# Kernel tuning notes

Hardware: AMD Instinct MI355X
Metric: run time of the kernel (lower is better)

## Reference

```python
import jax, jax.numpy as jnp
import numpy as np

B, L, D, H = 2, 2048, 1024, 16
DH = D // H
TAU = 0.1


def setup_inputs() -> dict:
    key = jax.random.key(0)
    ks = jax.random.split(key, 12)
    s = 0.02
    return {
        "q_x": jax.random.normal(ks[0], (B, L, D), jnp.float32),
        "k_x": jax.random.normal(ks[1], (B, L, D), jnp.float32),
        "v_x": jax.random.normal(ks[2], (B, L, D), jnp.float32),
        "ec": jax.random.normal(ks[3], (B, L, D), jnp.float32),
        "Wq": jax.random.normal(ks[4], (D, D), jnp.float32) * s,
        "bq": jnp.zeros((D,), jnp.float32),
        "Wk": jax.random.normal(ks[5], (D, D), jnp.float32) * s,
        "bk": jnp.zeros((D,), jnp.float32),
        "Wv": jax.random.normal(ks[6], (D, D), jnp.float32) * s,
        "bv": jnp.zeros((D,), jnp.float32),
        "Wo": jax.random.normal(ks[7], (D, D), jnp.float32) * s,
        "bo": jnp.zeros((D,), jnp.float32),
    }


def reference(q_x, k_x, v_x, ec, Wq, bq, Wk, bk, Wv, bv, Wo, bo):
    # torch nn.Linear: y = x @ W.T + b
    Q = (q_x @ Wq.T + bq).reshape(B, L, H, DH).transpose(0, 2, 1, 3)   # [B,H,L,Dh]
    K = (k_x @ Wk.T + bk).reshape(B, -1, H, DH).transpose(0, 2, 1, 3)  # [B,H,S,Dh]
    V = (v_x @ Wv.T + bv).reshape(B, -1, H, DH).transpose(0, 2, 1, 3)  # [B,H,S,Dh]
    scores = jnp.einsum("bhld,bhsd->bhls", Q, K) / jnp.sqrt(jnp.float32(DH))
    w = jnp.nan_to_num(jax.nn.softmax(scores, axis=-1), nan=0.0)       # [B,H,L,S]
    # frequency gate per key position: sigmoid((mean|ec| - tau) * 10)
    gate = jax.nn.sigmoid((jnp.abs(ec).mean(-1) - TAU) * 10.0)          # [B,S]
    w = w * gate[:, None, None, :]
    out = jnp.einsum("bhls,bhsd->bhld", w, V)                           # [B,H,L,Dh]
    out = out.transpose(0, 2, 1, 3).reshape(B, L, D)
    return out @ Wo.T + bo
```

## Files before the change

kernel.cpp:

```cpp
#include <hip/hip_runtime.h>

typedef unsigned short u16;
typedef unsigned int u32;
typedef unsigned long long u64;
typedef __attribute__((ext_vector_type(8))) short bf16x8;
typedef __attribute__((ext_vector_type(4))) float f32x4;
typedef __attribute__((ext_vector_type(2))) unsigned int u32x2;
typedef __attribute__((ext_vector_type(4))) unsigned int u32x4;

#define B_ 2
#define L_ 2048
#define D_ 1024
#define H_ 16
#define M_ 4096

__device__ __forceinline__ u16 f2bf(float f) {
  u32 x = __builtin_bit_cast(u32, f);
  return (u16)((x + 0x7fffu + ((x >> 16) & 1u)) >> 16);
}
__device__ __forceinline__ u32 cvtpk(float lo, float hi) {
  u32 r;
  asm("v_cvt_pk_bf16_f32 %0, %1, %2" : "=v"(r) : "v"(lo), "v"(hi));
  return r;
}

__device__ __forceinline__ void lane_regroup(u32& a, u32& b) {
#if __has_builtin(__builtin_amdgcn_permlane32_swap) && \
    __has_builtin(__builtin_amdgcn_permlane16_swap)
  u32x2 r = __builtin_amdgcn_permlane32_swap(a, b, false, false);
  u32x2 t = __builtin_amdgcn_permlane16_swap(r.x, r.y, false, false);
  a = t.x;
  b = t.y;
#else
  asm("v_permlane32_swap_b32 %0, %1\n\t"
      "v_permlane16_swap_b32 %0, %1"
      : "+v"(a), "+v"(b));
#endif
}

__device__ __forceinline__ void gl2lds16(void* lds, const void* g) {
  __builtin_amdgcn_global_load_lds(
      (const __attribute__((address_space(1))) u32*)g,
      (__attribute__((address_space(3))) u32*)lds, 16, 0, 0);
}

__device__ __forceinline__ void wait_vm8() {
  asm volatile("s_waitcnt vmcnt(8)" ::: "memory");
}
__device__ __forceinline__ void wait_vm0() {
  asm volatile("s_waitcnt vmcnt(0)" ::: "memory");
}
__device__ __forceinline__ void bar() {
  asm volatile("" ::: "memory");
  __builtin_amdgcn_s_barrier();
  asm volatile("" ::: "memory");
}

__global__ void cvt_all(const float* __restrict__ q, const float* __restrict__ k,
                        const float* __restrict__ v, const float* __restrict__ wq,
                        const float* __restrict__ wk, const float* __restrict__ wv,
                        const float* __restrict__ wo, u16* __restrict__ Xq,
                        u16* __restrict__ Xk, u16* __restrict__ Xv, u16* __restrict__ Wqb,
                        u16* __restrict__ Wkb, u16* __restrict__ Wvb,
                        u16* __restrict__ Wob) {
  int i = blockIdx.x * 256 + threadIdx.x;
  const float* s;
  u16* d;
  int off;
  if (i < 3145728) {
    int t = i >> 20;
    off = i & 1048575;
    s = t == 0 ? q : t == 1 ? k : v;
    d = t == 0 ? Xq : t == 1 ? Xk : Xv;
  } else {
    int j = i - 3145728;
    int t = j >> 18;
    off = j & 262143;
    s = t == 0 ? wq : t == 1 ? wk : t == 2 ? wv : wo;
    d = t == 0 ? Wqb : t == 1 ? Wkb : t == 2 ? Wvb : Wob;
  }
  float4 vv = ((const float4*)s)[off];
  ((u64*)d)[off] = (u64)cvtpk(vv.x, vv.y) | ((u64)cvtpk(vv.z, vv.w) << 32);
}

__global__ void gate_kernel(const float* __restrict__ ec, float* __restrict__ gate) {
  int row = blockIdx.x * 4 + (threadIdx.x >> 6);
  int lane = threadIdx.x & 63;
  const float4* p = (const float4*)(ec + (size_t)row * 1024);
  float s = 0.f;
#pragma unroll
  for (int i = 0; i < 4; i++) {
    float4 v = p[i * 64 + lane];
    s += fabsf(v.x) + fabsf(v.y) + fabsf(v.z) + fabsf(v.w);
  }
#pragma unroll
  for (int m = 1; m < 64; m <<= 1) s += __shfl_xor(s, m);
  if (lane == 0) {
    float mean = s * (1.0f / 1024.0f);
    gate[row] = 1.0f / (1.0f + __expf(-(mean - 0.1f) * 10.0f));
  }
}

__global__ __launch_bounds__(256, 2) void gemm_qkv(
    const u16* __restrict__ Xq, const u16* __restrict__ Xk, const u16* __restrict__ Xv,
    const u16* __restrict__ Wq, const u16* __restrict__ Wk, const u16* __restrict__ Wv,
    const float* __restrict__ bq, const float* __restrict__ bk,
    const float* __restrict__ bv, const float* __restrict__ gate,
    u16* __restrict__ Qo, u16* __restrict__ Ko, u16* __restrict__ Vt) {
  __shared__ char smem[65536];
  const int which = blockIdx.x >> 8;
  const u16* A = which == 0 ? Xq : which == 1 ? Xk : Xv;
  const u16* Bw = which == 0 ? Wq : which == 1 ? Wk : Wv;
  const float* bias = which == 0 ? bq : which == 1 ? bk : bv;
  const int bi = blockIdx.x & 255;
  const int tid = threadIdx.x;
  const int tm = bi >> 3;
  const int tn = bi & 7;
  const int w = tid >> 6, lane = tid & 63;
  const int c = lane & 15, g = lane >> 4;
  const int wr = (w >> 1) << 6, wc = (w & 1) << 6;
  const int srow = tid >> 3, sch = tid & 7;

  f32x4 acc[4][4] = {};

  auto stage = [&](int buf, int t) {
    char* As = smem + buf * 32768;
    char* Bs = As + 16384;
#pragma unroll
    for (int i = 0; i < 4; i++) {
      int row = i * 32 + srow;
      int chs = (sch ^ (row & 7)) << 3;
      gl2lds16(As + i * 4096 + w * 1024, A + (size_t)(tm * 128 + row) * 1024 + t * 64 + chs);
      gl2lds16(Bs + i * 4096 + w * 1024, Bw + (size_t)(tn * 128 + row) * 1024 + t * 64 + chs);
    }
  };

  stage(0, 0);
  for (int t = 0; t < 16; t++) {
    int cur = t & 1;
    if (t < 15) {
      stage(cur ^ 1, t + 1);
      wait_vm8();
    } else {
      wait_vm0();
    }
    bar();
    const char* As = smem + cur * 32768;
    const char* Bs = As + 16384;
#pragma unroll
    for (int kd = 0; kd < 2; kd++) {
      bf16x8 af[4], bfr[4];
#pragma unroll
      for (int fi = 0; fi < 4; fi++) {
        int ra = wr + fi * 16 + c;
        af[fi] = *(const bf16x8*)(As + ra * 128 + ((((kd << 2) | g) ^ (ra & 7)) << 4));
        int rb = wc + fi * 16 + c;
        bfr[fi] = *(const bf16x8*)(Bs + rb * 128 + ((((kd << 2) | g) ^ (rb & 7)) << 4));
      }
#pragma unroll
      for (int fi = 0; fi < 4; fi++)
#pragma unroll
        for (int fj = 0; fj < 4; fj++)
          acc[fi][fj] = __builtin_amdgcn_mfma_f32_16x16x32_bf16(af[fi], bfr[fj],
                                                                acc[fi][fj], 0, 0, 0);
    }
    bar();
  }

  if (which == 2) {
    u16* T = (u16*)smem;
    __syncthreads();
#pragma unroll
    for (int fi = 0; fi < 4; fi++) {
      int lr0 = wr + fi * 16 + g * 4;
      float4 gg = *(const float4*)(gate + tm * 128 + lr0);
#pragma unroll
      for (int fj = 0; fj < 4; fj++) {
        int lc = wc + fj * 16 + c;
        float bv2 = bias[tn * 128 + lc];
        T[lc * 136 + lr0 + 0] = f2bf((acc[fi][fj][0] + bv2) * gg.x);
        T[lc * 136 + lr0 + 1] = f2bf((acc[fi][fj][1] + bv2) * gg.y);
        T[lc * 136 + lr0 + 2] = f2bf((acc[fi][fj][2] + bv2) * gg.z);
        T[lc * 136 + lr0 + 3] = f2bf((acc[fi][fj][3] + bv2) * gg.w);
      }
    }
    __syncthreads();
    const int lc = tid >> 1, hf = tid & 1;
    const int vtrow = (tm >> 4) * 1024 + tn * 128 + lc;
    const int s0 = (tm & 15) * 128 + hf * 64;
    const char* Trow = (const char*)(T + lc * 136) + hf * 128;
    u16* dst = Vt + (size_t)vtrow * 2048 + s0;
#pragma unroll
    for (int j = 0; j < 8; j++)
      *(bf16x8*)(dst + j * 8) = *(const bf16x8*)(Trow + j * 16);
  } else {
    u16* Cout = which == 0 ? Qo : Ko;
    const int rowb = tm * 128 + wr + g * 4;
    const int colb = tn * 128 + wc + c;
#pragma unroll
    for (int fj = 0; fj < 4; fj++) {
      int col = colb + fj * 16;
      float bv2 = bias[col];
#pragma unroll
      for (int fi = 0; fi < 4; fi++) {
        int r0 = rowb + fi * 16;
#pragma unroll
        for (int r = 0; r < 4; r++)
          Cout[(size_t)(r0 + r) * 1024 + col] = f2bf(acc[fi][fj][r] + bv2);
      }
    }
  }
}

__global__ __launch_bounds__(256, 2) void gemm_o(const u16* __restrict__ A,
                                                 const u16* __restrict__ Bw,
                                                 const float* __restrict__ bias,
                                                 float* __restrict__ Cout) {
  __shared__ char smem[65536];
  const int tid = threadIdx.x;
  const int tm = blockIdx.x >> 3;
  const int tn = blockIdx.x & 7;
  const int w = tid >> 6, lane = tid & 63;
  const int c = lane & 15, g = lane >> 4;
  const int wr = (w >> 1) << 6, wc = (w & 1) << 6;
  const int srow = tid >> 3, sch = tid & 7;

  f32x4 acc[4][4] = {};

  auto stage = [&](int buf, int t) {
    char* As = smem + buf * 32768;
    char* Bs = As + 16384;
#pragma unroll
    for (int i = 0; i < 4; i++) {
      int row = i * 32 + srow;
      int chs = (sch ^ (row & 7)) << 3;
      gl2lds16(As + i * 4096 + w * 1024, A + (size_t)(tm * 128 + row) * 1024 + t * 64 + chs);
      gl2lds16(Bs + i * 4096 + w * 1024, Bw + (size_t)(tn * 128 + row) * 1024 + t * 64 + chs);
    }
  };

  stage(0, 0);
  for (int t = 0; t < 16; t++) {
    int cur = t & 1;
    if (t < 15) {
      stage(cur ^ 1, t + 1);
      wait_vm8();
    } else {
      wait_vm0();
    }
    bar();
    const char* As = smem + cur * 32768;
    const char* Bs = As + 16384;
#pragma unroll
    for (int kd = 0; kd < 2; kd++) {
      bf16x8 af[4], bfr[4];
#pragma unroll
      for (int fi = 0; fi < 4; fi++) {
        int ra = wr + fi * 16 + c;
        af[fi] = *(const bf16x8*)(As + ra * 128 + ((((kd << 2) | g) ^ (ra & 7)) << 4));
        int rb = wc + fi * 16 + c;
        bfr[fi] = *(const bf16x8*)(Bs + rb * 128 + ((((kd << 2) | g) ^ (rb & 7)) << 4));
      }
#pragma unroll
      for (int fi = 0; fi < 4; fi++)
#pragma unroll
        for (int fj = 0; fj < 4; fj++)
          acc[fi][fj] = __builtin_amdgcn_mfma_f32_16x16x32_bf16(af[fi], bfr[fj],
                                                                acc[fi][fj], 0, 0, 0);
    }
    bar();
  }

  const int rowb = tm * 128 + wr + g * 4;
  const int colb = tn * 128 + wc + c;
#pragma unroll
  for (int fj = 0; fj < 4; fj++) {
    int col = colb + fj * 16;
    float bv2 = bias[col];
#pragma unroll
    for (int fi = 0; fi < 4; fi++) {
      int r0 = rowb + fi * 16;
#pragma unroll
      for (int r = 0; r < 4; r++)
        Cout[(size_t)(r0 + r) * 1024 + col] = acc[fi][fj][r] + bv2;
    }
  }
}

__global__ __launch_bounds__(256, 2) void attn_kernel(const u16* __restrict__ Qb,
                                                      const u16* __restrict__ Kb,
                                                      const u16* __restrict__ Vt,
                                                      u16* __restrict__ Ob) {
  __shared__ char asmem[65536];
  const int bi = blockIdx.x;
  const int bh = (bi & 7) | ((bi >> 7) << 3);
  const int qt = (bi >> 3) & 15;
  const int b = bh >> 4, h = bh & 15;
  const int tid = threadIdx.x, w = tid >> 6, lane = tid & 63;
  const int c = lane & 15, g = lane >> 4;
  const int qrow0 = b * L_ + qt * 128 + w * 32;
  const float SCL = 0.18033688011112042f;

  bf16x8 qf[2][2];
#pragma unroll
  for (int fj = 0; fj < 2; fj++)
#pragma unroll
    for (int kd = 0; kd < 2; kd++)
      qf[fj][kd] = *(const bf16x8*)(Qb + (size_t)(qrow0 + fj * 16 + c) * D_ + h * 64 +
                                    kd * 32 + g * 8);

  float lsum[2] = {0.f, 0.f};
  f32x4 oacc[4][2] = {};

  const int srow = tid >> 3, sch = tid & 7;
  const int vrow = tid >> 4, vch = tid & 15;

  auto stage = [&](int buf, int kv) {
    char* KsB = asmem + buf * 32768;
    char* VsB = KsB + 16384;
    int sbase = kv * 128;
#pragma unroll
    for (int i = 0; i < 4; i++) {
      int kr = i * 32 + srow;
      gl2lds16(KsB + i * 4096 + w * 1024,
               Kb + (size_t)(b * L_ + sbase + kr) * D_ + h * 64 + ((sch ^ (kr & 7)) << 3));
      int vr = i * 16 + vrow;
      gl2lds16(VsB + i * 4096 + w * 1024,
               Vt + (size_t)(bh * 64 + vr) * 2048 + sbase + ((vch ^ (vr & 15)) << 3));
    }
  };

  stage(0, 0);
  for (int kv = 0; kv < 16; kv++) {
    int cur = kv & 1;
    if (kv < 15) {
      stage(cur ^ 1, kv + 1);
      wait_vm8();
    } else {
      wait_vm0();
    }
    bar();
    const char* Ks = asmem + cur * 32768;
    const char* Vs = Ks + 16384;

#pragma unroll
    for (int fj = 0; fj < 2; fj++) {
      f32x4 st[8] = {};
#pragma unroll
      for (int kd = 0; kd < 2; kd++) {
#pragma unroll
        for (int fi = 0; fi < 8; fi++) {
          int row = fi * 16 + c;
          bf16x8 kf = *(const bf16x8*)(Ks + row * 128 + ((((kd << 2) | g) ^ (c & 7)) << 4));
          st[fi] = __builtin_amdgcn_mfma_f32_16x16x32_bf16(kf, qf[fj][kd], st[fi], 0, 0, 0);
        }
      }
      float rs = 0.f;
      u32 pkA[8], pkB[8];
#pragma unroll
      for (int fi = 0; fi < 8; fi++) {
        float p0 = __builtin_amdgcn_exp2f(st[fi][0] * SCL);
        float p1 = __builtin_amdgcn_exp2f(st[fi][1] * SCL);
        float p2 = __builtin_amdgcn_exp2f(st[fi][2] * SCL);
        float p3 = __builtin_amdgcn_exp2f(st[fi][3] * SCL);
        rs += (p0 + p1) + (p2 + p3);
        pkA[fi] = cvtpk(p0, p1);
        pkB[fi] = cvtpk(p2, p3);
      }
      rs += __shfl_xor(rs, 16);
      rs += __shfl_xor(rs, 32);
      lsum[fj] += rs;
#pragma unroll
      for (int ks = 0; ks < 4; ks++) {
        u32 a0 = pkA[2 * ks], b0 = pkA[2 * ks + 1];
        lane_regroup(a0, b0);
        u32 a1 = pkB[2 * ks], b1 = pkB[2 * ks + 1];
        lane_regroup(a1, b1);
        u32x4 pw = {a0, a1, b0, b1};
        bf16x8 pf = __builtin_bit_cast(bf16x8, pw);
#pragma unroll
        for (int fd = 0; fd < 4; fd++) {
          int vr2 = fd * 16 + c;
          bf16x8 vf = *(const bf16x8*)(Vs + vr2 * 256 + ((((ks << 2) | g) ^ (vr2 & 15)) << 4));
          oacc[fd][fj] = __builtin_amdgcn_mfma_f32_16x16x32_bf16(vf, pf, oacc[fd][fj],
                                                                 0, 0, 0);
        }
      }
    }
    bar();
  }

#pragma unroll
  for (int fj = 0; fj < 2; fj++) {
    float inv = 1.0f / lsum[fj];
    size_t orow = (size_t)(qrow0 + fj * 16 + c) * D_ + h * 64;
#pragma unroll
    for (int fd = 0; fd < 4; fd++) {
      u64 pk = (u64)cvtpk(oacc[fd][fj][0] * inv, oacc[fd][fj][1] * inv) |
               ((u64)cvtpk(oacc[fd][fj][2] * inv, oacc[fd][fj][3] * inv) << 32);
      *(u64*)(Ob + orow + fd * 16 + g * 4) = pk;
    }
  }
}

extern "C" void kernel_launch(void* const* d_in, const int* in_sizes, int n_in,
                              void* d_out, int out_size, void* d_ws, size_t ws_size,
                              hipStream_t stream) {
  const float* q_x = (const float*)d_in[0];
  const float* k_x = (const float*)d_in[1];
  const float* v_x = (const float*)d_in[2];
  const float* ec = (const float*)d_in[3];
  const float* Wq = (const float*)d_in[4];
  const float* bq = (const float*)d_in[5];
  const float* Wk = (const float*)d_in[6];
  const float* bk = (const float*)d_in[7];
  const float* Wv = (const float*)d_in[8];
  const float* bv = (const float*)d_in[9];
  const float* Wo = (const float*)d_in[10];
  const float* bo = (const float*)d_in[11];

  char* ws = (char*)d_ws;
  const size_t MB = 1024 * 1024;
  u16* Wqb = (u16*)(ws + 0 * MB);
  u16* Wkb = (u16*)(ws + 2 * MB);
  u16* Wvb = (u16*)(ws + 4 * MB);
  u16* Wob = (u16*)(ws + 6 * MB);
  float* gatep = (float*)(ws + 8 * MB);
  u16* Xq = (u16*)(ws + 9 * MB);
  u16* Xk = (u16*)(ws + 17 * MB);
  u16* Xv = (u16*)(ws + 25 * MB);
  u16* Qb = (u16*)(ws + 33 * MB);
  u16* Kb = (u16*)(ws + 41 * MB);
  u16* Vtb = (u16*)(ws + 49 * MB);
  u16* Ab = Xk;

  gate_kernel<<<1024, 256, 0, stream>>>(ec, gatep);
  cvt_all<<<16384, 256, 0, stream>>>(q_x, k_x, v_x, Wq, Wk, Wv, Wo, Xq, Xk, Xv, Wqb,
                                     Wkb, Wvb, Wob);
  gemm_qkv<<<768, 256, 0, stream>>>(Xq, Xk, Xv, Wqb, Wkb, Wvb, bq, bk, bv, gatep, Qb,
                                    Kb, Vtb);
  attn_kernel<<<512, 256, 0, stream>>>(Qb, Kb, Vtb, Ab);
  gemm_o<<<256, 256, 0, stream>>>(Ab, Wob, bo, (float*)d_out);
}
```

Baseline: 120.2 us.

## Shrink attention tiles to 64x64 and fold softmax scale into Q projection

The attention kernel now gives each wave 16 query rows instead of 32 and streams 64-key tiles instead of 128. Shared memory halves to 32KB and the grid doubles to 1024 blocks, with launch bounds raised to 4 blocks per CU to improve occupancy and latency hiding. The softmax scale (log2e/sqrt(dh)) is now applied in the Q projection epilogue, which removes a multiply per score element in the attention loop. Costs: K/V tiles are reloaded twice as often per query row, there are more barriers per unit of work, and Q is rounded to bf16 after scaling.

```diff
diff --git a/kernel.cpp b/kernel.cpp
--- a/kernel.cpp
+++ b/kernel.cpp
@@ -46,6 +46,9 @@
 
 __device__ __forceinline__ void wait_vm8() {
   asm volatile("s_waitcnt vmcnt(8)" ::: "memory");
+}
+__device__ __forceinline__ void wait_vm4() {
+  asm volatile("s_waitcnt vmcnt(4)" ::: "memory");
 }
 __device__ __forceinline__ void wait_vm0() {
   asm volatile("s_waitcnt vmcnt(0)" ::: "memory");
@@ -195,6 +198,7 @@
       *(bf16x8*)(dst + j * 8) = *(const bf16x8*)(Trow + j * 16);
   } else {
     u16* Cout = which == 0 ? Qo : Ko;
+    const float oscl = which == 0 ? 0.18033688011112042f : 1.0f;
     const int rowb = tm * 128 + wr + g * 4;
     const int colb = tn * 128 + wc + c;
 #pragma unroll
@@ -206,7 +210,7 @@
         int r0 = rowb + fi * 16;
 #pragma unroll
         for (int r = 0; r < 4; r++)
-          Cout[(size_t)(r0 + r) * 1024 + col] = f2bf(acc[fi][fj][r] + bv2);
+          Cout[(size_t)(r0 + r) * 1024 + col] = f2bf((acc[fi][fj][r] + bv2) * oscl);
       }
     }
   }
@@ -287,119 +291,106 @@
   }
 }
 
-__global__ __launch_bounds__(256, 2) void attn_kernel(const u16* __restrict__ Qb,
+__global__ __launch_bounds__(256, 4) void attn_kernel(const u16* __restrict__ Qb,
                                                       const u16* __restrict__ Kb,
                                                       const u16* __restrict__ Vt,
                                                       u16* __restrict__ Ob) {
-  __shared__ char asmem[65536];
+  __shared__ char asmem[32768];
   const int bi = blockIdx.x;
-  const int bh = (bi & 7) | ((bi >> 7) << 3);
-  const int qt = (bi >> 3) & 15;
+  const int bh = (bi & 7) | ((bi >> 8) << 3);
+  const int qt = (bi >> 3) & 31;
   const int b = bh >> 4, h = bh & 15;
   const int tid = threadIdx.x, w = tid >> 6, lane = tid & 63;
   const int c = lane & 15, g = lane >> 4;
-  const int qrow0 = b * L_ + qt * 128 + w * 32;
-  const float SCL = 0.18033688011112042f;
-
-  bf16x8 qf[2][2];
-#pragma unroll
-  for (int fj = 0; fj < 2; fj++)
-#pragma unroll
-    for (int kd = 0; kd < 2; kd++)
-      qf[fj][kd] = *(const bf16x8*)(Qb + (size_t)(qrow0 + fj * 16 + c) * D_ + h * 64 +
-                                    kd * 32 + g * 8);
-
-  float lsum[2] = {0.f, 0.f};
-  f32x4 oacc[4][2] = {};
-
-  const int srow = tid >> 3, sch = tid & 7;
-  const int vrow = tid >> 4, vch = tid & 15;
+  const int qrow0 = b * L_ + qt * 64 + w * 16;
+
+  bf16x8 qf[2];
+#pragma unroll
+  for (int kd = 0; kd < 2; kd++)
+    qf[kd] = *(const bf16x8*)(Qb + (size_t)(qrow0 + c) * D_ + h * 64 + kd * 32 + g * 8);
+
+  float lsum = 0.f;
+  f32x4 oacc[4] = {};
+
+  const int lr = lane >> 3, lch = lane & 7;
 
   auto stage = [&](int buf, int kv) {
-    char* KsB = asmem + buf * 32768;
-    char* VsB = KsB + 16384;
-    int sbase = kv * 128;
-#pragma unroll
-    for (int i = 0; i < 4; i++) {
-      int kr = i * 32 + srow;
+    char* KsB = asmem + buf * 16384;
+    char* VsB = KsB + 8192;
+    int sbase = kv * 64;
+#pragma unroll
+    for (int i = 0; i < 2; i++) {
+      int kr = i * 32 + w * 8 + lr;
       gl2lds16(KsB + i * 4096 + w * 1024,
-               Kb + (size_t)(b * L_ + sbase + kr) * D_ + h * 64 + ((sch ^ (kr & 7)) << 3));
-      int vr = i * 16 + vrow;
+               Kb + (size_t)(b * L_ + sbase + kr) * D_ + h * 64 + ((lch ^ (kr & 7)) << 3));
       gl2lds16(VsB + i * 4096 + w * 1024,
-               Vt + (size_t)(bh * 64 + vr) * 2048 + sbase + ((vch ^ (vr & 15)) << 3));
+               Vt + (size_t)(bh * 64 + kr) * 2048 + sbase + ((lch ^ (kr & 7)) << 3));
     }
   };
 
   stage(0, 0);
-  for (int kv = 0; kv < 16; kv++) {
+  for (int kv = 0; kv < 32; kv++) {
     int cur = kv & 1;
-    if (kv < 15) {
+    if (kv < 31) {
       stage(cur ^ 1, kv + 1);
-      wait_vm8();
+      wait_vm4();
     } else {
       wait_vm0();
     }
     bar();
-    const char* Ks = asmem + cur * 32768;
-    const char* Vs = Ks + 16384;
-
-#pragma unroll
-    for (int fj = 0; fj < 2; fj++) {
-      f32x4 st[8] = {};
-#pragma unroll
-      for (int kd = 0; kd < 2; kd++) {
-#pragma unroll
-        for (int fi = 0; fi < 8; fi++) {
-          int row = fi * 16 + c;
-          bf16x8 kf = *(const bf16x8*)(Ks + row * 128 + ((((kd << 2) | g) ^ (c & 7)) << 4));
-          st[fi] = __builtin_amdgcn_mfma_f32_16x16x32_bf16(kf, qf[fj][kd], st[fi], 0, 0, 0);
-        }
-      }
-      float rs = 0.f;
-      u32 pkA[8], pkB[8];
-#pragma unroll
-      for (int fi = 0; fi < 8; fi++) {
-        float p0 = __builtin_amdgcn_exp2f(st[fi][0] * SCL);
-        float p1 = __builtin_amdgcn_exp2f(st[fi][1] * SCL);
-        float p2 = __builtin_amdgcn_exp2f(st[fi][2] * SCL);
-        float p3 = __builtin_amdgcn_exp2f(st[fi][3] * SCL);
-        rs += (p0 + p1) + (p2 + p3);
-        pkA[fi] = cvtpk(p0, p1);
-        pkB[fi] = cvtpk(p2, p3);
-      }
-      rs += __shfl_xor(rs, 16);
-      rs += __shfl_xor(rs, 32);
-      lsum[fj] += rs;
-#pragma unroll
-      for (int ks = 0; ks < 4; ks++) {
-        u32 a0 = pkA[2 * ks], b0 = pkA[2 * ks + 1];
-        lane_regroup(a0, b0);
-        u32 a1 = pkB[2 * ks], b1 = pkB[2 * ks + 1];
-        lane_regroup(a1, b1);
-        u32x4 pw = {a0, a1, b0, b1};
-        bf16x8 pf = __builtin_bit_cast(bf16x8, pw);
-#pragma unroll
-        for (int fd = 0; fd < 4; fd++) {
-          int vr2 = fd * 16 + c;
-          bf16x8 vf = *(const bf16x8*)(Vs + vr2 * 256 + ((((ks << 2) | g) ^ (vr2 & 15)) << 4));
-          oacc[fd][fj] = __builtin_amdgcn_mfma_f32_16x16x32_bf16(vf, pf, oacc[fd][fj],
-                                                                 0, 0, 0);
-        }
-      }
-    }
-    bar();
-  }
-
-#pragma unroll
-  for (int fj = 0; fj < 2; fj++) {
-    float inv = 1.0f / lsum[fj];
-    size_t orow = (size_t)(qrow0 + fj * 16 + c) * D_ + h * 64;
-#pragma unroll
-    for (int fd = 0; fd < 4; fd++) {
-      u64 pk = (u64)cvtpk(oacc[fd][fj][0] * inv, oacc[fd][fj][1] * inv) |
-               ((u64)cvtpk(oacc[fd][fj][2] * inv, oacc[fd][fj][3] * inv) << 32);
-      *(u64*)(Ob + orow + fd * 16 + g * 4) = pk;
-    }
+    const char* Ks = asmem + cur * 16384;
+    const char* Vs = Ks + 8192;
+
+    f32x4 st[4] = {};
+#pragma unroll
+    for (int kd = 0; kd < 2; kd++) {
+#pragma unroll
+      for (int fi = 0; fi < 4; fi++) {
+        int row = fi * 16 + c;
+        bf16x8 kf = *(const bf16x8*)(Ks + row * 128 + ((((kd << 2) | g) ^ (c & 7)) << 4));
+        st[fi] = __builtin_amdgcn_mfma_f32_16x16x32_bf16(kf, qf[kd], st[fi], 0, 0, 0);
+      }
+    }
+    float rs = 0.f;
+    u32 pkA[4], pkB[4];
+#pragma unroll
+    for (int fi = 0; fi < 4; fi++) {
+      float p0 = __builtin_amdgcn_exp2f(st[fi][0]);
+      float p1 = __builtin_amdgcn_exp2f(st[fi][1]);
+      float p2 = __builtin_amdgcn_exp2f(st[fi][2]);
+      float p3 = __builtin_amdgcn_exp2f(st[fi][3]);
+      rs += (p0 + p1) + (p2 + p3);
+      pkA[fi] = cvtpk(p0, p1);
+      pkB[fi] = cvtpk(p2, p3);
+    }
+    rs += __shfl_xor(rs, 16);
+    rs += __shfl_xor(rs, 32);
+    lsum += rs;
+#pragma unroll
+    for (int ks = 0; ks < 2; ks++) {
+      u32 a0 = pkA[2 * ks], b0 = pkA[2 * ks + 1];
+      lane_regroup(a0, b0);
+      u32 a1 = pkB[2 * ks], b1 = pkB[2 * ks + 1];
+      lane_regroup(a1, b1);
+      u32x4 pw = {a0, a1, b0, b1};
+      bf16x8 pf = __builtin_bit_cast(bf16x8, pw);
+#pragma unroll
+      for (int fd = 0; fd < 4; fd++) {
+        int vr2 = fd * 16 + c;
+        bf16x8 vf = *(const bf16x8*)(Vs + vr2 * 128 + ((((ks << 2) | g) ^ (c & 7)) << 4));
+        oacc[fd] = __builtin_amdgcn_mfma_f32_16x16x32_bf16(vf, pf, oacc[fd], 0, 0, 0);
+      }
+    }
+    bar();
+  }
+
+  float inv = 1.0f / lsum;
+  size_t orow = (size_t)(qrow0 + c) * D_ + h * 64;
+#pragma unroll
+  for (int fd = 0; fd < 4; fd++) {
+    u64 pk = (u64)cvtpk(oacc[fd][0] * inv, oacc[fd][1] * inv) |
+             ((u64)cvtpk(oacc[fd][2] * inv, oacc[fd][3] * inv) << 32);
+    *(u64*)(Ob + orow + fd * 16 + g * 4) = pk;
   }
 }
 
@@ -439,6 +430,6 @@
                                      Wkb, Wvb, Wob);
   gemm_qkv<<<768, 256, 0, stream>>>(Xq, Xk, Xv, Wqb, Wkb, Wvb, bq, bk, bv, gatep, Qb,
                                     Kb, Vtb);
-  attn_kernel<<<512, 256, 0, stream>>>(Qb, Kb, Vtb, Ab);
+  attn_kernel<<<1024, 256, 0, stream>>>(Qb, Kb, Vtb, Ab);
   gemm_o<<<256, 256, 0, stream>>>(Ab, Wob, bo, (float*)d_out);
 }
```

Result: slower. 124.6 us (+3.6%).

## Fuse gate into conversion kernel, fold softmax scale into Q, share K fragments

Applied to the files above, without the earlier changes.

Merges the gate reduction into the conversion launch as extra blocks, removing one kernel launch. Pre-multiplies Q by the softmax scale in the QKV GEMM epilogue, so the attention loop no longer multiplies every score. The attention loop now computes QK^T for both query fragments together, reusing each K LDS read and raising MFMA priority during that phase. The trade-off is that both score tiles are live at once, which raises register pressure, and Q is rounded to bf16 after scaling.

```diff
diff --git a/kernel.cpp b/kernel.cpp
--- a/kernel.cpp
+++ b/kernel.cpp
@@ -59,10 +59,29 @@
 __global__ void cvt_all(const float* __restrict__ q, const float* __restrict__ k,
                         const float* __restrict__ v, const float* __restrict__ wq,
                         const float* __restrict__ wk, const float* __restrict__ wv,
-                        const float* __restrict__ wo, u16* __restrict__ Xq,
-                        u16* __restrict__ Xk, u16* __restrict__ Xv, u16* __restrict__ Wqb,
-                        u16* __restrict__ Wkb, u16* __restrict__ Wvb,
-                        u16* __restrict__ Wob) {
+                        const float* __restrict__ wo, const float* __restrict__ ec,
+                        u16* __restrict__ Xq, u16* __restrict__ Xk, u16* __restrict__ Xv,
+                        u16* __restrict__ Wqb, u16* __restrict__ Wkb,
+                        u16* __restrict__ Wvb, u16* __restrict__ Wob,
+                        float* __restrict__ gate) {
+  if (blockIdx.x >= 16384) {
+    int row = (blockIdx.x - 16384) * 4 + (threadIdx.x >> 6);
+    int lane = threadIdx.x & 63;
+    const float4* p = (const float4*)(ec + (size_t)row * 1024);
+    float s = 0.f;
+#pragma unroll
+    for (int i = 0; i < 4; i++) {
+      float4 vv = p[i * 64 + lane];
+      s += fabsf(vv.x) + fabsf(vv.y) + fabsf(vv.z) + fabsf(vv.w);
+    }
+#pragma unroll
+    for (int m = 1; m < 64; m <<= 1) s += __shfl_xor(s, m);
+    if (lane == 0) {
+      float mean = s * (1.0f / 1024.0f);
+      gate[row] = 1.0f / (1.0f + __expf(-(mean - 0.1f) * 10.0f));
+    }
+    return;
+  }
   int i = blockIdx.x * 256 + threadIdx.x;
   const float* s;
   u16* d;
@@ -81,24 +100,6 @@
   }
   float4 vv = ((const float4*)s)[off];
   ((u64*)d)[off] = (u64)cvtpk(vv.x, vv.y) | ((u64)cvtpk(vv.z, vv.w) << 32);
-}
-
-__global__ void gate_kernel(const float* __restrict__ ec, float* __restrict__ gate) {
-  int row = blockIdx.x * 4 + (threadIdx.x >> 6);
-  int lane = threadIdx.x & 63;
-  const float4* p = (const float4*)(ec + (size_t)row * 1024);
-  float s = 0.f;
-#pragma unroll
-  for (int i = 0; i < 4; i++) {
-    float4 v = p[i * 64 + lane];
-    s += fabsf(v.x) + fabsf(v.y) + fabsf(v.z) + fabsf(v.w);
-  }
-#pragma unroll
-  for (int m = 1; m < 64; m <<= 1) s += __shfl_xor(s, m);
-  if (lane == 0) {
-    float mean = s * (1.0f / 1024.0f);
-    gate[row] = 1.0f / (1.0f + __expf(-(mean - 0.1f) * 10.0f));
-  }
 }
 
 __global__ __launch_bounds__(256, 2) void gemm_qkv(
@@ -195,6 +196,7 @@
       *(bf16x8*)(dst + j * 8) = *(const bf16x8*)(Trow + j * 16);
   } else {
     u16* Cout = which == 0 ? Qo : Ko;
+    const float oscl = which == 0 ? 0.18033688011112042f : 1.0f;
     const int rowb = tm * 128 + wr + g * 4;
     const int colb = tn * 128 + wc + c;
 #pragma unroll
@@ -206,7 +208,7 @@
         int r0 = rowb + fi * 16;
 #pragma unroll
         for (int r = 0; r < 4; r++)
-          Cout[(size_t)(r0 + r) * 1024 + col] = f2bf(acc[fi][fj][r] + bv2);
+          Cout[(size_t)(r0 + r) * 1024 + col] = f2bf((acc[fi][fj][r] + bv2) * oscl);
       }
     }
   }
@@ -287,6 +289,39 @@
   }
 }
 
+#define SMPV(ST, FJ)                                                                   \
+  do {                                                                                 \
+    float rs_ = 0.f;                                                                   \
+    u32 pkA_[8], pkB_[8];                                                              \
+    _Pragma("unroll") for (int fi = 0; fi < 8; fi++) {                                 \
+      float p0 = __builtin_amdgcn_exp2f(ST[fi][0]);                                    \
+      float p1 = __builtin_amdgcn_exp2f(ST[fi][1]);                                    \
+      float p2 = __builtin_amdgcn_exp2f(ST[fi][2]);                                    \
+      float p3 = __builtin_amdgcn_exp2f(ST[fi][3]);                                    \
+      rs_ += (p0 + p1) + (p2 + p3);                                                    \
+      pkA_[fi] = cvtpk(p0, p1);                                                        \
+      pkB_[fi] = cvtpk(p2, p3);                                                        \
+    }                                                                                  \
+    rs_ += __shfl_xor(rs_, 16);                                                        \
+    rs_ += __shfl_xor(rs_, 32);                                                        \
+    lsum[FJ] += rs_;                                                                   \
+    _Pragma("unroll") for (int ks = 0; ks < 4; ks++) {                                 \
+      u32 a0 = pkA_[2 * ks], b0 = pkA_[2 * ks + 1];                                    \
+      lane_regroup(a0, b0);                                                            \
+      u32 a1 = pkB_[2 * ks], b1 = pkB_[2 * ks + 1];                                    \
+      lane_regroup(a1, b1);                                                            \
+      u32x4 pw = {a0, a1, b0, b1};                                                     \
+      bf16x8 pf = __builtin_bit_cast(bf16x8, pw);                                      \
+      _Pragma("unroll") for (int fd = 0; fd < 4; fd++) {                               \
+        int vr2 = fd * 16 + c;                                                         \
+        bf16x8 vf = *(const bf16x8*)(Vs + vr2 * 256 +                                  \
+                                     ((((ks << 2) | g) ^ (vr2 & 15)) << 4));           \
+        oacc[fd][FJ] =                                                                 \
+            __builtin_amdgcn_mfma_f32_16x16x32_bf16(vf, pf, oacc[fd][FJ], 0, 0, 0);    \
+      }                                                                                \
+    }                                                                                  \
+  } while (0)
+
 __global__ __launch_bounds__(256, 2) void attn_kernel(const u16* __restrict__ Qb,
                                                       const u16* __restrict__ Kb,
                                                       const u16* __restrict__ Vt,
@@ -299,7 +334,6 @@
   const int tid = threadIdx.x, w = tid >> 6, lane = tid & 63;
   const int c = lane & 15, g = lane >> 4;
   const int qrow0 = b * L_ + qt * 128 + w * 32;
-  const float SCL = 0.18033688011112042f;
 
   bf16x8 qf[2][2];
 #pragma unroll
@@ -343,50 +377,21 @@
     const char* Ks = asmem + cur * 32768;
     const char* Vs = Ks + 16384;
 
-#pragma unroll
-    for (int fj = 0; fj < 2; fj++) {
-      f32x4 st[8] = {};
-#pragma unroll
-      for (int kd = 0; kd < 2; kd++) {
-#pragma unroll
-        for (int fi = 0; fi < 8; fi++) {
-          int row = fi * 16 + c;
-          bf16x8 kf = *(const bf16x8*)(Ks + row * 128 + ((((kd << 2) | g) ^ (c & 7)) << 4));
-          st[fi] = __builtin_amdgcn_mfma_f32_16x16x32_bf16(kf, qf[fj][kd], st[fi], 0, 0, 0);
-        }
+    f32x4 st0[8] = {}, st1[8] = {};
+    __builtin_amdgcn_s_setprio(1);
+#pragma unroll
+    for (int kd = 0; kd < 2; kd++) {
+#pragma unroll
+      for (int fi = 0; fi < 8; fi++) {
+        int row = fi * 16 + c;
+        bf16x8 kf = *(const bf16x8*)(Ks + row * 128 + ((((kd << 2) | g) ^ (c & 7)) << 4));
+        st0[fi] = __builtin_amdgcn_mfma_f32_16x16x32_bf16(kf, qf[0][kd], st0[fi], 0, 0, 0);
+        st1[fi] = __builtin_amdgcn_mfma_f32_16x16x32_bf16(kf, qf[1][kd], st1[fi], 0, 0, 0);
       }
-      float rs = 0.f;
-      u32 pkA[8], pkB[8];
-#pragma unroll
-      for (int fi = 0; fi < 8; fi++) {
-        float p0 = __builtin_amdgcn_exp2f(st[fi][0] * SCL);
-        float p1 = __builtin_amdgcn_exp2f(st[fi][1] * SCL);
-        float p2 = __builtin_amdgcn_exp2f(st[fi][2] * SCL);
-        float p3 = __builtin_amdgcn_exp2f(st[fi][3] * SCL);
-        rs += (p0 + p1) + (p2 + p3);
-        pkA[fi] = cvtpk(p0, p1);
-        pkB[fi] = cvtpk(p2, p3);
-      }
-      rs += __shfl_xor(rs, 16);
-      rs += __shfl_xor(rs, 32);
-      lsum[fj] += rs;
-#pragma unroll
-      for (int ks = 0; ks < 4; ks++) {
-        u32 a0 = pkA[2 * ks], b0 = pkA[2 * ks + 1];
-        lane_regroup(a0, b0);
-        u32 a1 = pkB[2 * ks], b1 = pkB[2 * ks + 1];
-        lane_regroup(a1, b1);
-        u32x4 pw = {a0, a1, b0, b1};
-        bf16x8 pf = __builtin_bit_cast(bf16x8, pw);
-#pragma unroll
-        for (int fd = 0; fd < 4; fd++) {
-          int vr2 = fd * 16 + c;
-          bf16x8 vf = *(const bf16x8*)(Vs + vr2 * 256 + ((((ks << 2) | g) ^ (vr2 & 15)) << 4));
-          oacc[fd][fj] = __builtin_amdgcn_mfma_f32_16x16x32_bf16(vf, pf, oacc[fd][fj],
-                                                                 0, 0, 0);
-        }
-      }
-    }
+    }
+    __builtin_amdgcn_s_setprio(0);
+    SMPV(st0, 0);
+    SMPV(st1, 1);
     bar();
   }
 
@@ -434,9 +439,8 @@
   u16* Vtb = (u16*)(ws + 49 * MB);
   u16* Ab = Xk;
 
-  gate_kernel<<<1024, 256, 0, stream>>>(ec, gatep);
-  cvt_all<<<16384, 256, 0, stream>>>(q_x, k_x, v_x, Wq, Wk, Wv, Wo, Xq, Xk, Xv, Wqb,
-                                     Wkb, Wvb, Wob);
+  cvt_all<<<17408, 256, 0, stream>>>(q_x, k_x, v_x, Wq, Wk, Wv, Wo, ec, Xq, Xk, Xv,
+                                     Wqb, Wkb, Wvb, Wob, gatep);
   gemm_qkv<<<768, 256, 0, stream>>>(Xq, Xk, Xv, Wqb, Wkb, Wvb, bq, bk, bv, gatep, Qb,
                                     Kb, Vtb);
   attn_kernel<<<512, 256, 0, stream>>>(Qb, Kb, Vtb, Ab);
```

Result: faster. 117.2 us (-2.6%).
